# Performance work log

Hardware: AMD Instinct MI355X
Metric: run time of the kernel (lower is better)

Reference implementation:

```python
import jax, jax.numpy as jnp
import numpy as np

B, N, F, D, M, R, K, TOPR = 32, 1024, 10, 64, 4, 8, 20, 2
TAU = 1.0
BN_EPS = 1e-5


def setup_inputs() -> dict:
    key = jax.random.key(0)
    ks = jax.random.split(key, 20)
    s = 0.1
    p = {}
    p['data'] = jax.random.normal(ks[0], (B, N, F), jnp.float32)
    u = jnp.clip(jax.random.uniform(ks[1], (B, M), jnp.float32), 1e-6, 1.0 - 1e-6)
    p['gumbel_noise'] = -jnp.log(-jnp.log(u))
    p['W_cond'] = jax.random.normal(ks[2], (F, D), jnp.float32) * s
    p['b_cond'] = jnp.zeros((D,), jnp.float32)
    p['W_ap'] = jax.random.normal(ks[3], (D, D), jnp.float32) * s
    p['b_ap'] = jnp.zeros((D,), jnp.float32)
    p['W_av'] = jax.random.normal(ks[4], (D, 1), jnp.float32) * s
    p['W_r'] = jax.random.normal(ks[5], (D, M), jnp.float32) * s
    p['b_r'] = jnp.zeros((M,), jnp.float32)
    p['e_base'] = jax.random.normal(ks[6], (N, D), jnp.float32) * s
    p['lr_u'] = jax.random.normal(ks[7], (M, N, R), jnp.float32) * s
    p['lr_v'] = jax.random.normal(ks[8], (M, R, D), jnp.float32) * s
    p['W_gnn'] = jax.random.normal(ks[9], (F, D), jnp.float32) * s
    p['att_i'] = jax.random.normal(ks[10], (D,), jnp.float32) * s
    p['att_j'] = jax.random.normal(ks[11], (D,), jnp.float32) * s
    p['att_em_i'] = jax.random.normal(ks[12], (D,), jnp.float32) * s
    p['att_em_j'] = jax.random.normal(ks[13], (D,), jnp.float32) * s
    p['b_gnn'] = jnp.zeros((D,), jnp.float32)
    p['bn1_gamma'] = jnp.ones((D,), jnp.float32)
    p['bn1_beta'] = jnp.zeros((D,), jnp.float32)
    p['node_embed_table'] = jax.random.normal(ks[14], (N, D), jnp.float32) * s
    p['bn_out_gamma'] = jnp.ones((D,), jnp.float32)
    p['bn_out_beta'] = jnp.zeros((D,), jnp.float32)
    p['W_out'] = jax.random.normal(ks[15], (D, 1), jnp.float32) * s
    p['b_out'] = jnp.zeros((1,), jnp.float32)
    return p


def _nan(x):
    return jnp.nan_to_num(x, nan=0.0, posinf=1e4, neginf=-1e4)


def _bn(x, gamma, beta, axes):
    # BatchNorm1d in training mode: biased batch stats over `axes`.
    mu = x.mean(axes, keepdims=True)
    var = x.var(axes, keepdims=True)
    return (x - mu) * jax.lax.rsqrt(var + BN_EPS) * gamma + beta


def reference(data, gumbel_noise, W_cond, b_cond, W_ap, b_ap, W_av, W_r, b_r,
              e_base, lr_u, lr_v, W_gnn, att_i, att_j, att_em_i, att_em_j,
              b_gnn, bn1_gamma, bn1_beta, node_embed_table,
              bn_out_gamma, bn_out_beta, W_out, b_out):
    x_det = jax.lax.stop_gradient(data)                      # data.clone().detach()
    # --- condition attention pooling ---
    h_it = data @ W_cond + b_cond                            # [B,N,D]
    ah = jax.nn.leaky_relu(h_it @ W_ap + b_ap, 0.2)
    e_it = _nan((ah @ W_av)[..., 0])                         # [B,N]
    beta = jax.nn.softmax(e_it, axis=1)
    h_sys = jnp.sum(beta[..., None] * h_it, axis=1)          # [B,D]
    # --- gumbel top-k routing with straight-through ---
    pi_soft = jax.nn.softmax((h_sys @ W_r + b_r + gumbel_noise) / TAU, axis=-1)
    topv, topi = jax.lax.top_k(pi_soft, TOPR)
    pi_hard = jnp.sum(jax.nn.one_hot(topi, M, dtype=pi_soft.dtype) * topv[..., None], axis=1)
    pi_hard = pi_hard / jnp.maximum(pi_hard.sum(-1, keepdims=True), 1e-12)
    pi_t = jax.lax.stop_gradient(pi_hard - pi_soft) + pi_soft
    # --- low-rank expert prototypes -> mixed node embeddings ---
    proto = e_base[None] + jnp.einsum('mnr,mrd->mnd', lr_u, lr_v)    # [M,N,D]
    mixed = _nan(jnp.einsum('bm,mnd->bnd', pi_t, proto))             # [B,N,D]
    # --- dynamic top-k graph construction ---
    scores = _nan(jnp.einsum('bid,bjd->bij', mixed, mixed))          # [B,N,N]
    topk_vals, topk_idx = jax.lax.top_k(scores, K)                   # src nodes per dst: [B,N,K]
    topk_w = jax.nn.softmax(topk_vals, axis=-1)                      # edge weights
    # --- GAT-style layer with embedding-augmented keys, self loops re-added ---
    x_lin = x_det @ W_gnn                                            # [B,N,D]
    s_i = x_lin @ att_i + mixed @ att_em_i                           # [B,N]
    s_j = x_lin @ att_j + mixed @ att_em_j
    sj_nb = jnp.take_along_axis(s_j, topk_idx.reshape(B, N * K), axis=1).reshape(B, N, K)
    self_mask = topk_idx == jnp.arange(N)[None, :, None]             # remove_self_loops on topk edges
    alpha_nb = jnp.where(self_mask, -jnp.inf, jax.nn.leaky_relu(s_i[:, :, None] + sj_nb, 0.2))
    alpha_self = jax.nn.leaky_relu(s_i + s_j, 0.2)
    att = jax.nn.softmax(jnp.concatenate([alpha_nb, alpha_self[..., None]], axis=-1), axis=-1)
    w_nb = att[..., :K] * topk_w                                     # edge_weight modulation
    w_self = att[..., K]
    x_src = jnp.take_along_axis(x_lin, topk_idx.reshape(B, N * K)[..., None], axis=1).reshape(B, N, K, D)
    gnn = jnp.einsum('bnk,bnkd->bnd', w_nb, x_src) + w_self[..., None] * x_lin + b_gnn
    gnn = jax.nn.relu(_bn(gnn.reshape(B * N, D), bn1_gamma, bn1_beta, 0).reshape(B, N, D))
    # --- output head ---
    out = gnn * node_embed_table[None]                               # [B,N,D]
    out = jax.nn.relu(_bn(out, bn_out_gamma, bn_out_beta, (0, 1)))   # dropout = identity (eval)
    out = (out @ W_out + b_out).reshape(-1, N)                       # [B,N]
    return out, h_sys, pi_soft
```

## Files before the change

### kernel.cpp

```cpp
#include <hip/hip_runtime.h>
#include <math.h>

#define BB 32
#define NN 1024
#define FF 10
#define DD 64
#define MM 4
#define RR 8
#define KK 20
#define BNROWS (BB*NN)

#define OFF_HIT   0ull
#define OFF_XLIN  2097152ull
#define OFF_EIT   4194304ull
#define OFF_PIT   4227072ull
#define OFF_MIXED 4227200ull
#define OFF_SI    6324352ull
#define OFF_SJ    6357120ull
#define OFF_GNN   7700608ull
#define OFF_OUTP  9797760ull
#define OFF_STAT  11894912ull

__device__ __forceinline__ float wave_sum(float v) {
    #pragma unroll
    for (int off = 32; off; off >>= 1) v += __shfl_xor(v, off);
    return v;
}
__device__ __forceinline__ float wave_max(float v) {
    #pragma unroll
    for (int off = 32; off; off >>= 1) v = fmaxf(v, __shfl_xor(v, off));
    return v;
}

__global__ __launch_bounds__(256) void k_rows(
    const float* __restrict__ data, const float* __restrict__ W_cond,
    const float* __restrict__ b_cond, const float* __restrict__ W_ap,
    const float* __restrict__ b_ap, const float* __restrict__ W_av,
    const float* __restrict__ W_gnn,
    float* __restrict__ h_it, float* __restrict__ x_lin, float* __restrict__ e_it,
    float* __restrict__ stats)
{
    if (blockIdx.x < 10) {
        int idx = blockIdx.x * 256 + threadIdx.x;
        if (idx < 2336) stats[idx] = 0.f;
    }
    int w = threadIdx.x >> 6, lane = threadIdx.x & 63;
    int r = blockIdx.x * 4 + w;
    const float* dr = data + r * FF;
    float df[FF];
    #pragma unroll
    for (int f = 0; f < FF; f++) df[f] = dr[f];
    float h = b_cond[lane], x = 0.f;
    #pragma unroll
    for (int f = 0; f < FF; f++) {
        h = fmaf(df[f], W_cond[f * DD + lane], h);
        x = fmaf(df[f], W_gnn[f * DD + lane], x);
    }
    h_it[r * DD + lane] = h;
    x_lin[r * DD + lane] = x;
    float acc = b_ap[lane];
    #pragma unroll
    for (int e2 = 0; e2 < DD; e2++)
        acc = fmaf(__shfl(h, e2), W_ap[e2 * DD + lane], acc);
    float lr = acc > 0.f ? acc : 0.2f * acc;
    float ep = wave_sum(lr * W_av[lane]);
    if (lane == 0) e_it[r] = ep;
}

__global__ __launch_bounds__(256) void k_pool2(
    const float* __restrict__ e_it, const float* __restrict__ h_it,
    float* __restrict__ num, float* __restrict__ den)
{
    int w = threadIdx.x >> 6, lane = threadIdx.x & 63;
    int b = blockIdx.x >> 3, ch = blockIdx.x & 7;
    int base = b * NN + ch * 128 + w * 32;
    float acc = 0.f, dn = 0.f;
    #pragma unroll 4
    for (int i = 0; i < 32; i++) {
        float e = e_it[base + i];
        float wgt = expf(e);
        acc = fmaf(wgt, h_it[(size_t)(base + i) * DD + lane], acc);
        dn += wgt;
    }
    __shared__ float pa[4][DD];
    __shared__ float pd[4];
    pa[w][lane] = acc;
    if (lane == 0) pd[w] = dn;
    __syncthreads();
    if (w == 0) {
        float s = pa[0][lane] + pa[1][lane] + pa[2][lane] + pa[3][lane];
        atomicAdd(&num[b * DD + lane], s);
        if (lane == 0) atomicAdd(&den[b], pd[0] + pd[1] + pd[2] + pd[3]);
    }
}

__global__ void k_route(const float* __restrict__ num, const float* __restrict__ den,
                        const float* __restrict__ W_r, const float* __restrict__ b_r,
                        const float* __restrict__ gumbel,
                        float* __restrict__ h_sys, float* __restrict__ pi_soft,
                        float* __restrict__ pi_t)
{
    int tid = threadIdx.x;
    for (int i = tid; i < BB * DD; i += 256)
        h_sys[i] = num[i] / den[i >> 6];
    if (tid >= BB) return;
    int b = tid;
    float inv = 1.0f / den[b];
    float lg[MM];
    #pragma unroll
    for (int m = 0; m < MM; m++) lg[m] = b_r[m] + gumbel[b * MM + m];
    for (int d = 0; d < DD; d++) {
        float hv = num[b * DD + d] * inv;
        #pragma unroll
        for (int m = 0; m < MM; m++) lg[m] = fmaf(hv, W_r[d * MM + m], lg[m]);
    }
    float mx = fmaxf(fmaxf(lg[0], lg[1]), fmaxf(lg[2], lg[3]));
    float s = 0.f, p[MM];
    #pragma unroll
    for (int m = 0; m < MM; m++) { p[m] = expf(lg[m] - mx); s += p[m]; }
    #pragma unroll
    for (int m = 0; m < MM; m++) { p[m] /= s; pi_soft[b * MM + m] = p[m]; }
    int i1 = 0; float v1 = p[0];
    #pragma unroll
    for (int m = 1; m < MM; m++) if (p[m] > v1) { v1 = p[m]; i1 = m; }
    int i2 = -1; float v2 = -1.f;
    #pragma unroll
    for (int m = 0; m < MM; m++) if (m != i1 && p[m] > v2) { v2 = p[m]; i2 = m; }
    float norm = fmaxf(v1 + v2, 1e-12f);
    #pragma unroll
    for (int m = 0; m < MM; m++)
        pi_t[b * MM + m] = (m == i1 ? v1 : (m == i2 ? v2 : 0.f)) / norm;
}

__global__ __launch_bounds__(256) void k_mixed(
    const float* __restrict__ e_base, const float* __restrict__ lr_u,
    const float* __restrict__ lr_v, const float* __restrict__ pi_t,
    const float* __restrict__ x_lin,
    const float* __restrict__ att_i, const float* __restrict__ att_j,
    const float* __restrict__ att_em_i, const float* __restrict__ att_em_j,
    float* __restrict__ mixed, float* __restrict__ s_i, float* __restrict__ s_j)
{
    int w = threadIdx.x >> 6, lane = threadIdx.x & 63;
    int r = blockIdx.x * 4 + w;
    int b = r >> 10, n = r & 1023;
    float LR[MM];
    #pragma unroll
    for (int m = 0; m < MM; m++) {
        float a = 0.f;
        #pragma unroll
        for (int rr = 0; rr < RR; rr++)
            a = fmaf(lr_u[(m * NN + n) * RR + rr], lr_v[(m * RR + rr) * DD + lane], a);
        LR[m] = a;
    }
    float eb = e_base[n * DD + lane];
    float mx = 0.f;
    #pragma unroll
    for (int m = 0; m < MM; m++) mx = fmaf(pi_t[b * MM + m], eb + LR[m], mx);
    mixed[(size_t)r * DD + lane] = mx;
    float x = x_lin[(size_t)r * DD + lane];
    float r1 = wave_sum(x * att_i[lane] + mx * att_em_i[lane]);
    float r2 = wave_sum(x * att_j[lane] + mx * att_em_j[lane]);
    if (lane == 0) { s_i[r] = r1; s_j[r] = r2; }
}

__global__ __launch_bounds__(512) void k_fused(
    const float* __restrict__ mixed, const float* __restrict__ x_lin,
    const float* __restrict__ s_i, const float* __restrict__ s_j,
    const float* __restrict__ b_gnn, float* __restrict__ gnn_pre,
    float* __restrict__ stats)
{
    __shared__ float As[32 * DD];
    __shared__ float BT[DD * 256];

    int t = threadIdx.x;
    int w = t >> 6, lane = t & 63;
    int b = blockIdx.x >> 5;
    int it = blockIdx.x & 31;
    int i0 = it * 32;
    const float* mb = mixed + (size_t)b * NN * DD;

    *(float4*)&As[t * 4] = *(const float4*)(mb + (size_t)i0 * DD + t * 4);

    float acc[4][16];
    #pragma unroll
    for (int a = 0; a < 4; a++)
        #pragma unroll
        for (int s = 0; s < 16; s++) acc[a][s] = 0.f;

    int jl = t >> 1;
    int dh = (t & 1) * 32;
    int rbase = w * 4;

    const float4* BT4 = (const float4*)BT;
    const float4* As4 = (const float4*)As;

    #pragma unroll
    for (int c = 0; c < 4; c++) {
        __syncthreads();
        const float* src = mb + (size_t)(c * 256 + jl) * DD + dh;
        #pragma unroll
        for (int i = 0; i < 8; i++) {
            float4 v = *(const float4*)(src + i * 4);
            int d0 = dh + i * 4;
            BT[(d0 + 0) * 256 + jl] = v.x;
            BT[(d0 + 1) * 256 + jl] = v.y;
            BT[(d0 + 2) * 256 + jl] = v.z;
            BT[(d0 + 3) * 256 + jl] = v.w;
        }
        __syncthreads();
        #pragma unroll 4
        for (int d4 = 0; d4 < 16; d4++) {
            float4 b0 = BT4[(d4 * 4 + 0) * 64 + lane];
            float4 b1 = BT4[(d4 * 4 + 1) * 64 + lane];
            float4 b2 = BT4[(d4 * 4 + 2) * 64 + lane];
            float4 b3 = BT4[(d4 * 4 + 3) * 64 + lane];
            #pragma unroll
            for (int rr = 0; rr < 4; rr++) {
                float4 a = As4[(rbase + rr) * 16 + d4];
                acc[rr][c * 4 + 0] = fmaf(a.w, b3.x, fmaf(a.z, b2.x, fmaf(a.y, b1.x, fmaf(a.x, b0.x, acc[rr][c * 4 + 0]))));
                acc[rr][c * 4 + 1] = fmaf(a.w, b3.y, fmaf(a.z, b2.y, fmaf(a.y, b1.y, fmaf(a.x, b0.y, acc[rr][c * 4 + 1]))));
                acc[rr][c * 4 + 2] = fmaf(a.w, b3.z, fmaf(a.z, b2.z, fmaf(a.y, b1.z, fmaf(a.x, b0.z, acc[rr][c * 4 + 2]))));
                acc[rr][c * 4 + 3] = fmaf(a.w, b3.w, fmaf(a.z, b2.w, fmaf(a.y, b1.w, fmaf(a.x, b0.w, acc[rr][c * 4 + 3]))));
            }
        }
    }
    __syncthreads();

    unsigned* skeyW = (unsigned*)&BT[w * 64];
    int*      sjjW  = (int*)&BT[512 + w * 64];

    float ssum = 0.f, qsum = 0.f;

    #pragma unroll 1
    for (int rr = 0; rr < 4; rr++) {
        int n = i0 + rbase + rr;
        int r = (b << 10) + n;

        unsigned uk[16];
        #define EXTRACT_ROW(RRC) \
            _Pragma("unroll") \
            for (int s = 0; s < 16; s++) { \
                unsigned u = __float_as_uint(acc[RRC][s]); \
                uk[s] = u ^ (((unsigned)((int)u >> 31)) | 0x80000000u); \
            }
        if (rr == 0)      { EXTRACT_ROW(0) }
        else if (rr == 1) { EXTRACT_ROW(1) }
        else if (rr == 2) { EXTRACT_ROW(2) }
        else              { EXTRACT_ROW(3) }

        unsigned mx = uk[0];
        #pragma unroll
        for (int i = 1; i < 16; i++) mx = uk[i] > mx ? uk[i] : mx;
        unsigned sv = mx;
        #pragma unroll
        for (int blk = 2; blk <= 64; blk <<= 1) {
            #pragma unroll
            for (int dist = blk >> 1; dist >= 1; dist >>= 1) {
                unsigned pv = (unsigned)__shfl_xor((int)sv, dist);
                bool up = (lane & blk) == 0;
                bool upper = (lane & dist) == 0;
                bool gt = sv > pv;
                sv = ((gt == upper) == up) ? sv : pv;
            }
        }
        unsigned tau = (unsigned)__shfl((int)sv, 19);

        int base = 0;
        #pragma unroll
        for (int s = 0; s < 16; s++) {
            bool q = uk[s] >= tau;
            unsigned long long m = __ballot(q);
            if (q) {
                int pos = base + __popcll(m & ((1ull << lane) - 1ull));
                if (pos < 64) {
                    skeyW[pos] = uk[s];
                    sjjW[pos] = ((s >> 2) << 8) + lane * 4 + (s & 3);
                }
            }
            base += __popcll(m);
        }
        int C = base;

        float vk = -INFINITY; int ik = 0;
        if (C <= 64) {
            unsigned ck = 0u; int cj = 0x7FFFFFFF;
            if (lane < C) { ck = skeyW[lane]; cj = sjjW[lane]; }
            if (C <= 32) {
                #pragma unroll
                for (int blk = 2; blk <= 32; blk <<= 1)
                    #pragma unroll
                    for (int dist = blk >> 1; dist >= 1; dist >>= 1) {
                        unsigned pk = (unsigned)__shfl_xor((int)ck, dist);
                        int pj = __shfl_xor(cj, dist);
                        bool up = (lane & blk) == 0;
                        bool upper = (lane & dist) == 0;
                        bool gt = (ck > pk) || (ck == pk && cj < pj);
                        bool keep = ((gt == upper) == up);
                        ck = keep ? ck : pk; cj = keep ? cj : pj;
                    }
            } else {
                #pragma unroll
                for (int blk = 2; blk <= 64; blk <<= 1)
                    #pragma unroll
                    for (int dist = blk >> 1; dist >= 1; dist >>= 1) {
                        unsigned pk = (unsigned)__shfl_xor((int)ck, dist);
                        int pj = __shfl_xor(cj, dist);
                        bool up = (lane & blk) == 0;
                        bool upper = (lane & dist) == 0;
                        bool gt = (ck > pk) || (ck == pk && cj < pj);
                        bool keep = ((gt == upper) == up);
                        ck = keep ? ck : pk; cj = keep ? cj : pj;
                    }
            }
            if (lane < KK) {
                unsigned u = (ck & 0x80000000u) ? (ck ^ 0x80000000u) : ~ck;
                vk = __uint_as_float(u);
                ik = cj;
            }
        } else {
            for (int k = 0; k < KK; k++) {
                unsigned bm = uk[0]; int bsl = 0;
                #pragma unroll
                for (int i = 1; i < 16; i++) if (uk[i] > bm) { bm = uk[i]; bsl = i; }
                unsigned wm = bm;
                #pragma unroll
                for (int off = 32; off; off >>= 1) {
                    unsigned tt = (unsigned)__shfl_xor((int)wm, off);
                    wm = tt > wm ? tt : wm;
                }
                unsigned long long ball = __ballot(bm == wm);
                int winner = (int)__builtin_ctzll(ball);
                int slotw = __shfl(bsl, winner);
                int jw = ((slotw >> 2) << 8) + winner * 4 + (slotw & 3);
                unsigned u2 = (wm & 0x80000000u) ? (wm ^ 0x80000000u) : ~wm;
                if (lane == k) { vk = __uint_as_float(u2); ik = jw; }
                if (lane == winner) uk[bsl] = 0u;
            }
        }

        float m1 = wave_max(vk);
        float ek = (lane < KK) ? expf(vk - m1) : 0.f;
        float s1v = wave_sum(ek);
        float wk = ek / s1v;
        float si = s_i[r], sjn = s_j[r];
        float a = -INFINITY;
        if (lane < KK) {
            float sjk = s_j[(b << 10) + ik];
            float t2 = si + sjk;
            a = (ik == n) ? -INFINITY : (t2 > 0.f ? t2 : 0.2f * t2);
        }
        float ts = si + sjn;
        float aself = ts > 0.f ? ts : 0.2f * ts;
        float am = wave_max(fmaxf(a, aself));
        float ea = (lane < KK && a != -INFINITY) ? expf(a - am) : 0.f;
        float es = expf(aself - am);
        float sm = wave_sum(ea) + es;
        float wnb = (ea / sm) * wk;
        float wself = es / sm;
        float gacc = b_gnn[lane] + wself * x_lin[(size_t)r * DD + lane];
        #pragma unroll
        for (int k = 0; k < KK; k++) {
            int jk = __shfl(ik, k);
            float wv = __shfl(wnb, k);
            gacc = fmaf(wv, x_lin[((size_t)(b << 10) + jk) * DD + lane], gacc);
        }
        gnn_pre[(size_t)r * DD + lane] = gacc;
        ssum += gacc;
        qsum = fmaf(gacc, gacc, qsum);
    }

    float* ps = &BT[1024];
    float* pq = &BT[1536];
    ps[w * 64 + lane] = ssum;
    pq[w * 64 + lane] = qsum;
    __syncthreads();
    if (w == 0) {
        float s = 0.f, q2 = 0.f;
        #pragma unroll
        for (int k2 = 0; k2 < 8; k2++) { s += ps[k2 * 64 + lane]; q2 += pq[k2 * 64 + lane]; }
        atomicAdd(&stats[lane], s);
        atomicAdd(&stats[DD + lane], q2);
    }
}

__global__ __launch_bounds__(256) void k_bn1(
    const float* __restrict__ gnn_pre, float* __restrict__ stats,
    const float* __restrict__ gamma, const float* __restrict__ beta,
    const float* __restrict__ net, float* __restrict__ out_pre)
{
    int tid = threadIdx.x;
    int d0 = (tid & 15) * 4;
    float mean4[4], rs4[4], bt4[4];
    #pragma unroll
    for (int k = 0; k < 4; k++) {
        float mu = stats[d0 + k] * (1.0f / BNROWS);
        float var = stats[64 + d0 + k] * (1.0f / BNROWS) - mu * mu;
        mean4[k] = mu;
        rs4[k] = rsqrtf(var + 1e-5f) * gamma[d0 + k];
        bt4[k] = beta[d0 + k];
    }
    float s4[4] = {0, 0, 0, 0}, q4[4] = {0, 0, 0, 0};
    size_t base4 = (size_t)blockIdx.x * 2048;
    #pragma unroll
    for (int i = 0; i < 8; i++) {
        size_t f4 = base4 + (size_t)i * 256 + tid;
        float4 v = ((const float4*)gnn_pre)[f4];
        int n = ((int)(f4 >> 4)) & 1023;
        float4 nv = ((const float4*)net)[(size_t)n * 16 + (tid & 15)];
        float vv[4] = {v.x, v.y, v.z, v.w};
        float nn2[4] = {nv.x, nv.y, nv.z, nv.w};
        float ov[4];
        #pragma unroll
        for (int k = 0; k < 4; k++) {
            float y = (vv[k] - mean4[k]) * rs4[k] + bt4[k];
            y = y > 0.f ? y : 0.f;
            float o = y * nn2[k];
            ov[k] = o;
            s4[k] += o;
            q4[k] = fmaf(o, o, q4[k]);
        }
        float4 o4 = {ov[0], ov[1], ov[2], ov[3]};
        ((float4*)out_pre)[f4] = o4;
    }
    __shared__ float4 ls[256], lq[256];
    ls[tid] = make_float4(s4[0], s4[1], s4[2], s4[3]);
    lq[tid] = make_float4(q4[0], q4[1], q4[2], q4[3]);
    __syncthreads();
    if (tid < 16) {
        float4 S = ls[tid], Q = lq[tid];
        #pragma unroll
        for (int rr = 1; rr < 16; rr++) {
            float4 a = ls[tid + 16 * rr], b = lq[tid + 16 * rr];
            S.x += a.x; S.y += a.y; S.z += a.z; S.w += a.w;
            Q.x += b.x; Q.y += b.y; Q.z += b.z; Q.w += b.w;
        }
        atomicAdd(&stats[128 + tid * 4 + 0], S.x);
        atomicAdd(&stats[128 + tid * 4 + 1], S.y);
        atomicAdd(&stats[128 + tid * 4 + 2], S.z);
        atomicAdd(&stats[128 + tid * 4 + 3], S.w);
        atomicAdd(&stats[192 + tid * 4 + 0], Q.x);
        atomicAdd(&stats[192 + tid * 4 + 1], Q.y);
        atomicAdd(&stats[192 + tid * 4 + 2], Q.z);
        atomicAdd(&stats[192 + tid * 4 + 3], Q.w);
    }
}

__global__ __launch_bounds__(256) void k_head(
    const float* __restrict__ out_pre, const float* __restrict__ stats,
    const float* __restrict__ gamma, const float* __restrict__ beta,
    const float* __restrict__ W_out, const float* __restrict__ b_out,
    float* __restrict__ out)
{
    int w = threadIdx.x >> 6, lane = threadIdx.x & 63;
    int r = blockIdx.x * 4 + w;
    float mean = stats[lane] * (1.0f / BNROWS);
    float var = stats[DD + lane] * (1.0f / BNROWS) - mean * mean;
    float rs = rsqrtf(var + 1e-5f);
    float y = (out_pre[(size_t)r * DD + lane] - mean) * rs * gamma[lane] + beta[lane];
    y = y > 0.f ? y : 0.f;
    float p = wave_sum(y * W_out[lane]);
    if (lane == 0) out[r] = p + b_out[0];
}

extern "C" void kernel_launch(void* const* d_in, const int* in_sizes, int n_in,
                              void* d_out, int out_size, void* d_ws, size_t ws_size,
                              hipStream_t stream)
{
    const float* data     = (const float*)d_in[0];
    const float* gumbel   = (const float*)d_in[1];
    const float* W_cond   = (const float*)d_in[2];
    const float* b_cond   = (const float*)d_in[3];
    const float* W_ap     = (const float*)d_in[4];
    const float* b_ap     = (const float*)d_in[5];
    const float* W_av     = (const float*)d_in[6];
    const float* W_r      = (const float*)d_in[7];
    const float* b_r      = (const float*)d_in[8];
    const float* e_base   = (const float*)d_in[9];
    const float* lr_u     = (const float*)d_in[10];
    const float* lr_v     = (const float*)d_in[11];
    const float* W_gnn    = (const float*)d_in[12];
    const float* att_i    = (const float*)d_in[13];
    const float* att_j    = (const float*)d_in[14];
    const float* att_em_i = (const float*)d_in[15];
    const float* att_em_j = (const float*)d_in[16];
    const float* b_gnn    = (const float*)d_in[17];
    const float* bn1_g    = (const float*)d_in[18];
    const float* bn1_b    = (const float*)d_in[19];
    const float* net      = (const float*)d_in[20];
    const float* bno_g    = (const float*)d_in[21];
    const float* bno_b    = (const float*)d_in[22];
    const float* W_out    = (const float*)d_in[23];
    const float* b_out    = (const float*)d_in[24];

    float* ws = (float*)d_ws;
    float* h_it   = ws + OFF_HIT;
    float* x_lin  = ws + OFF_XLIN;
    float* e_it   = ws + OFF_EIT;
    float* pi_t   = ws + OFF_PIT;
    float* mixed  = ws + OFF_MIXED;
    float* s_i    = ws + OFF_SI;
    float* s_j    = ws + OFF_SJ;
    float* gnn_pre = ws + OFF_GNN;
    float* out_pre = ws + OFF_OUTP;
    float* stats   = ws + OFF_STAT;
    float* pnum    = stats + 256;
    float* pden    = stats + 2304;

    float* out0    = (float*)d_out;
    float* h_sys   = out0 + BB * NN;
    float* pi_soft = out0 + BB * NN + BB * DD;

    k_rows<<<BNROWS / 4, 256, 0, stream>>>(data, W_cond, b_cond, W_ap, b_ap, W_av, W_gnn,
                                           h_it, x_lin, e_it, stats);
    k_pool2<<<BB * 8, 256, 0, stream>>>(e_it, h_it, pnum, pden);
    k_route<<<1, 256, 0, stream>>>(pnum, pden, W_r, b_r, gumbel, h_sys, pi_soft, pi_t);
    k_mixed<<<BNROWS / 4, 256, 0, stream>>>(e_base, lr_u, lr_v, pi_t, x_lin,
                                            att_i, att_j, att_em_i, att_em_j, mixed, s_i, s_j);
    k_fused<<<BB * 32, 512, 0, stream>>>(mixed, x_lin, s_i, s_j, b_gnn, gnn_pre, stats);
    k_bn1<<<256, 256, 0, stream>>>(gnn_pre, stats, bn1_g, bn1_b, net, out_pre);
    k_head<<<BNROWS / 4, 256, 0, stream>>>(out_pre, stats + 128, bno_g, bno_b, W_out, b_out, out0);
}
```

Before: 373.6 us.

## Enlarge similarity tile to 64 rows and prefetch next B chunk in registers

```diff
diff --git a/kernel.cpp b/kernel.cpp
--- a/kernel.cpp
+++ b/kernel.cpp
@@ -163,44 +163,47 @@
     if (lane == 0) { s_i[r] = r1; s_j[r] = r2; }
 }
 
-__global__ __launch_bounds__(512) void k_fused(
+__global__ __launch_bounds__(512, 2) void k_fsg64(
     const float* __restrict__ mixed, const float* __restrict__ x_lin,
     const float* __restrict__ s_i, const float* __restrict__ s_j,
     const float* __restrict__ b_gnn, float* __restrict__ gnn_pre,
     float* __restrict__ stats)
 {
-    __shared__ float As[32 * DD];
     __shared__ float BT[DD * 256];
 
     int t = threadIdx.x;
     int w = t >> 6, lane = t & 63;
-    int b = blockIdx.x >> 5;
-    int it = blockIdx.x & 31;
-    int i0 = it * 32;
+    int b = blockIdx.x >> 4;
+    int it = blockIdx.x & 15;
+    int i0 = it * 64;
     const float* mb = mixed + (size_t)b * NN * DD;
 
-    *(float4*)&As[t * 4] = *(const float4*)(mb + (size_t)i0 * DD + t * 4);
-
-    float acc[4][16];
-    #pragma unroll
-    for (int a = 0; a < 4; a++)
+    float acc[8][16];
+    #pragma unroll
+    for (int a = 0; a < 8; a++)
         #pragma unroll
         for (int s = 0; s < 16; s++) acc[a][s] = 0.f;
 
     int jl = t >> 1;
     int dh = (t & 1) * 32;
-    int rbase = w * 4;
+    int rbase = w * 8;
+    const float* arow = mb + (size_t)(i0 + rbase) * DD;
 
     const float4* BT4 = (const float4*)BT;
-    const float4* As4 = (const float4*)As;
+
+    float4 pa[2][8];
+    {
+        const float* src = mb + (size_t)jl * DD + dh;
+        #pragma unroll
+        for (int i = 0; i < 8; i++) pa[0][i] = *(const float4*)(src + i * 4);
+    }
 
     #pragma unroll
     for (int c = 0; c < 4; c++) {
-        __syncthreads();
-        const float* src = mb + (size_t)(c * 256 + jl) * DD + dh;
+        if (c) __syncthreads();
         #pragma unroll
         for (int i = 0; i < 8; i++) {
-            float4 v = *(const float4*)(src + i * 4);
+            float4 v = pa[c & 1][i];
             int d0 = dh + i * 4;
             BT[(d0 + 0) * 256 + jl] = v.x;
             BT[(d0 + 1) * 256 + jl] = v.y;
@@ -208,6 +211,11 @@
             BT[(d0 + 3) * 256 + jl] = v.w;
         }
         __syncthreads();
+        if (c < 3) {
+            const float* src = mb + (size_t)((c + 1) * 256 + jl) * DD + dh;
+            #pragma unroll
+            for (int i = 0; i < 8; i++) pa[(c + 1) & 1][i] = *(const float4*)(src + i * 4);
+        }
         #pragma unroll 4
         for (int d4 = 0; d4 < 16; d4++) {
             float4 b0 = BT4[(d4 * 4 + 0) * 64 + lane];
@@ -215,8 +223,8 @@
             float4 b2 = BT4[(d4 * 4 + 2) * 64 + lane];
             float4 b3 = BT4[(d4 * 4 + 3) * 64 + lane];
             #pragma unroll
-            for (int rr = 0; rr < 4; rr++) {
-                float4 a = As4[(rbase + rr) * 16 + d4];
+            for (int rr = 0; rr < 8; rr++) {
+                float4 a = *(const float4*)(arow + (size_t)rr * DD + d4 * 4);
                 acc[rr][c * 4 + 0] = fmaf(a.w, b3.x, fmaf(a.z, b2.x, fmaf(a.y, b1.x, fmaf(a.x, b0.x, acc[rr][c * 4 + 0]))));
                 acc[rr][c * 4 + 1] = fmaf(a.w, b3.y, fmaf(a.z, b2.y, fmaf(a.y, b1.y, fmaf(a.x, b0.y, acc[rr][c * 4 + 1]))));
                 acc[rr][c * 4 + 2] = fmaf(a.w, b3.z, fmaf(a.z, b2.z, fmaf(a.y, b1.z, fmaf(a.x, b0.z, acc[rr][c * 4 + 2]))));
@@ -232,7 +240,7 @@
     float ssum = 0.f, qsum = 0.f;
 
     #pragma unroll 1
-    for (int rr = 0; rr < 4; rr++) {
+    for (int rr = 0; rr < 8; rr++) {
         int n = i0 + rbase + rr;
         int r = (b << 10) + n;
 
@@ -246,7 +254,11 @@
         if (rr == 0)      { EXTRACT_ROW(0) }
         else if (rr == 1) { EXTRACT_ROW(1) }
         else if (rr == 2) { EXTRACT_ROW(2) }
-        else              { EXTRACT_ROW(3) }
+        else if (rr == 3) { EXTRACT_ROW(3) }
+        else if (rr == 4) { EXTRACT_ROW(4) }
+        else if (rr == 5) { EXTRACT_ROW(5) }
+        else if (rr == 6) { EXTRACT_ROW(6) }
+        else              { EXTRACT_ROW(7) }
 
         unsigned mx = uk[0];
         #pragma unroll
@@ -516,7 +528,7 @@
     k_route<<<1, 256, 0, stream>>>(pnum, pden, W_r, b_r, gumbel, h_sys, pi_soft, pi_t);
     k_mixed<<<BNROWS / 4, 256, 0, stream>>>(e_base, lr_u, lr_v, pi_t, x_lin,
                                             att_i, att_j, att_em_i, att_em_j, mixed, s_i, s_j);
-    k_fused<<<BB * 32, 512, 0, stream>>>(mixed, x_lin, s_i, s_j, b_gnn, gnn_pre, stats);
+    k_fsg64<<<BB * 16, 512, 0, stream>>>(mixed, x_lin, s_i, s_j, b_gnn, gnn_pre, stats);
     k_bn1<<<256, 256, 0, stream>>>(gnn_pre, stats, bn1_g, bn1_b, net, out_pre);
     k_head<<<BNROWS / 4, 256, 0, stream>>>(out_pre, stats + 128, bno_g, bno_b, W_out, b_out, out0);
 }
```

Result: slower. 448.4 us (+20.0%).

## Restructure similarity GEMM tiling: smaller B tiles, A rows from global

Applied to the files above, without the earlier changes.

```diff
diff --git a/kernel.cpp b/kernel.cpp
--- a/kernel.cpp
+++ b/kernel.cpp
@@ -163,14 +163,13 @@
     if (lane == 0) { s_i[r] = r1; s_j[r] = r2; }
 }
 
-__global__ __launch_bounds__(512) void k_fused(
+__global__ __launch_bounds__(512) void k_fsg(
     const float* __restrict__ mixed, const float* __restrict__ x_lin,
     const float* __restrict__ s_i, const float* __restrict__ s_j,
     const float* __restrict__ b_gnn, float* __restrict__ gnn_pre,
     float* __restrict__ stats)
 {
-    __shared__ float As[32 * DD];
-    __shared__ float BT[DD * 256];
+    __shared__ float4 BT[16 * 128];
 
     int t = threadIdx.x;
     int w = t >> 6, lane = t & 63;
@@ -179,55 +178,64 @@
     int i0 = it * 32;
     const float* mb = mixed + (size_t)b * NN * DD;
 
-    *(float4*)&As[t * 4] = *(const float4*)(mb + (size_t)i0 * DD + t * 4);
-
     float acc[4][16];
     #pragma unroll
     for (int a = 0; a < 4; a++)
         #pragma unroll
         for (int s = 0; s < 16; s++) acc[a][s] = 0.f;
 
-    int jl = t >> 1;
-    int dh = (t & 1) * 32;
+    int js = t >> 2;
+    int dq = t & 3;
+    int wslot = ((js & 1) << 6) | (js >> 1);
     int rbase = w * 4;
-
-    const float4* BT4 = (const float4*)BT;
-    const float4* As4 = (const float4*)As;
-
-    #pragma unroll
-    for (int c = 0; c < 4; c++) {
+    const float* arow = mb + (size_t)(i0 + rbase) * DD;
+
+    #pragma unroll
+    for (int c = 0; c < 8; c++) {
+        if (c) __syncthreads();
+        {
+            const float* src = mb + (size_t)(c * 128 + js) * DD + dq * 16;
+            float4 pf0 = *(const float4*)(src);
+            float4 pf1 = *(const float4*)(src + 4);
+            float4 pf2 = *(const float4*)(src + 8);
+            float4 pf3 = *(const float4*)(src + 12);
+            BT[(dq * 4 + 0) * 128 + wslot] = pf0;
+            BT[(dq * 4 + 1) * 128 + wslot] = pf1;
+            BT[(dq * 4 + 2) * 128 + wslot] = pf2;
+            BT[(dq * 4 + 3) * 128 + wslot] = pf3;
+        }
         __syncthreads();
-        const float* src = mb + (size_t)(c * 256 + jl) * DD + dh;
-        #pragma unroll
-        for (int i = 0; i < 8; i++) {
-            float4 v = *(const float4*)(src + i * 4);
-            int d0 = dh + i * 4;
-            BT[(d0 + 0) * 256 + jl] = v.x;
-            BT[(d0 + 1) * 256 + jl] = v.y;
-            BT[(d0 + 2) * 256 + jl] = v.z;
-            BT[(d0 + 3) * 256 + jl] = v.w;
-        }
-        __syncthreads();
-        #pragma unroll 4
+        float4 ac0 = *(const float4*)(arow + 0 * DD);
+        float4 ac1 = *(const float4*)(arow + 1 * DD);
+        float4 ac2 = *(const float4*)(arow + 2 * DD);
+        float4 ac3 = *(const float4*)(arow + 3 * DD);
+        #pragma unroll 1
         for (int d4 = 0; d4 < 16; d4++) {
-            float4 b0 = BT4[(d4 * 4 + 0) * 64 + lane];
-            float4 b1 = BT4[(d4 * 4 + 1) * 64 + lane];
-            float4 b2 = BT4[(d4 * 4 + 2) * 64 + lane];
-            float4 b3 = BT4[(d4 * 4 + 3) * 64 + lane];
-            #pragma unroll
-            for (int rr = 0; rr < 4; rr++) {
-                float4 a = As4[(rbase + rr) * 16 + d4];
-                acc[rr][c * 4 + 0] = fmaf(a.w, b3.x, fmaf(a.z, b2.x, fmaf(a.y, b1.x, fmaf(a.x, b0.x, acc[rr][c * 4 + 0]))));
-                acc[rr][c * 4 + 1] = fmaf(a.w, b3.y, fmaf(a.z, b2.y, fmaf(a.y, b1.y, fmaf(a.x, b0.y, acc[rr][c * 4 + 1]))));
-                acc[rr][c * 4 + 2] = fmaf(a.w, b3.z, fmaf(a.z, b2.z, fmaf(a.y, b1.z, fmaf(a.x, b0.z, acc[rr][c * 4 + 2]))));
-                acc[rr][c * 4 + 3] = fmaf(a.w, b3.w, fmaf(a.z, b2.w, fmaf(a.y, b1.w, fmaf(a.x, b0.w, acc[rr][c * 4 + 3]))));
-            }
+            float4 b0 = BT[d4 * 128 + lane];
+            float4 b1 = BT[d4 * 128 + 64 + lane];
+            float4 an0, an1, an2, an3;
+            if (d4 < 15) {
+                an0 = *(const float4*)(arow + 0 * DD + (d4 + 1) * 4);
+                an1 = *(const float4*)(arow + 1 * DD + (d4 + 1) * 4);
+                an2 = *(const float4*)(arow + 2 * DD + (d4 + 1) * 4);
+                an3 = *(const float4*)(arow + 3 * DD + (d4 + 1) * 4);
+            }
+            acc[0][c*2+0] = fmaf(ac0.w, b0.w, fmaf(ac0.z, b0.z, fmaf(ac0.y, b0.y, fmaf(ac0.x, b0.x, acc[0][c*2+0]))));
+            acc[0][c*2+1] = fmaf(ac0.w, b1.w, fmaf(ac0.z, b1.z, fmaf(ac0.y, b1.y, fmaf(ac0.x, b1.x, acc[0][c*2+1]))));
+            acc[1][c*2+0] = fmaf(ac1.w, b0.w, fmaf(ac1.z, b0.z, fmaf(ac1.y, b0.y, fmaf(ac1.x, b0.x, acc[1][c*2+0]))));
+            acc[1][c*2+1] = fmaf(ac1.w, b1.w, fmaf(ac1.z, b1.z, fmaf(ac1.y, b1.y, fmaf(ac1.x, b1.x, acc[1][c*2+1]))));
+            acc[2][c*2+0] = fmaf(ac2.w, b0.w, fmaf(ac2.z, b0.z, fmaf(ac2.y, b0.y, fmaf(ac2.x, b0.x, acc[2][c*2+0]))));
+            acc[2][c*2+1] = fmaf(ac2.w, b1.w, fmaf(ac2.z, b1.z, fmaf(ac2.y, b1.y, fmaf(ac2.x, b1.x, acc[2][c*2+1]))));
+            acc[3][c*2+0] = fmaf(ac3.w, b0.w, fmaf(ac3.z, b0.z, fmaf(ac3.y, b0.y, fmaf(ac3.x, b0.x, acc[3][c*2+0]))));
+            acc[3][c*2+1] = fmaf(ac3.w, b1.w, fmaf(ac3.z, b1.z, fmaf(ac3.y, b1.y, fmaf(ac3.x, b1.x, acc[3][c*2+1]))));
+            ac0 = an0; ac1 = an1; ac2 = an2; ac3 = an3;
         }
     }
     __syncthreads();
 
-    unsigned* skeyW = (unsigned*)&BT[w * 64];
-    int*      sjjW  = (int*)&BT[512 + w * 64];
+    float* BTf = (float*)BT;
+    unsigned* skeyW = (unsigned*)&BTf[w * 64];
+    int*      sjjW  = (int*)&BTf[512 + w * 64];
 
     float ssum = 0.f, qsum = 0.f;
 
@@ -274,7 +282,7 @@
                 int pos = base + __popcll(m & ((1ull << lane) - 1ull));
                 if (pos < 64) {
                     skeyW[pos] = uk[s];
-                    sjjW[pos] = ((s >> 2) << 8) + lane * 4 + (s & 3);
+                    sjjW[pos] = ((s >> 1) << 7) + lane * 2 + (s & 1);
                 }
             }
             base += __popcll(m);
@@ -331,7 +339,7 @@
                 unsigned long long ball = __ballot(bm == wm);
                 int winner = (int)__builtin_ctzll(ball);
                 int slotw = __shfl(bsl, winner);
-                int jw = ((slotw >> 2) << 8) + winner * 4 + (slotw & 3);
+                int jw = ((slotw >> 1) << 7) + winner * 2 + (slotw & 1);
                 unsigned u2 = (wm & 0x80000000u) ? (wm ^ 0x80000000u) : ~wm;
                 if (lane == k) { vk = __uint_as_float(u2); ik = jw; }
                 if (lane == winner) uk[bsl] = 0u;
@@ -369,8 +377,8 @@
         qsum = fmaf(gacc, gacc, qsum);
     }
 
-    float* ps = &BT[1024];
-    float* pq = &BT[1536];
+    float* ps = &BTf[1024];
+    float* pq = &BTf[1536];
     ps[w * 64 + lane] = ssum;
     pq[w * 64 + lane] = qsum;
     __syncthreads();
@@ -516,7 +524,7 @@
     k_route<<<1, 256, 0, stream>>>(pnum, pden, W_r, b_r, gumbel, h_sys, pi_soft, pi_t);
     k_mixed<<<BNROWS / 4, 256, 0, stream>>>(e_base, lr_u, lr_v, pi_t, x_lin,
                                             att_i, att_j, att_em_i, att_em_j, mixed, s_i, s_j);
-    k_fused<<<BB * 32, 512, 0, stream>>>(mixed, x_lin, s_i, s_j, b_gnn, gnn_pre, stats);
+    k_fsg<<<BB * 32, 512, 0, stream>>>(mixed, x_lin, s_i, s_j, b_gnn, gnn_pre, stats);
     k_bn1<<<256, 256, 0, stream>>>(gnn_pre, stats, bn1_g, bn1_b, net, out_pre);
     k_head<<<BNROWS / 4, 256, 0, stream>>>(out_pre, stats + 128, bno_g, bno_b, W_out, b_out, out0);
 }
```

New measurement: 436.4 us. +16.8%, slower.
